# Kernel tuning notes

Hardware: AMD Instinct MI355X
Metric: run time of the kernel (lower is better)

Reference implementation:

```python
import jax, jax.numpy as jnp
import numpy as np

B, N, C = 2, 2048, 1024
H, HD = 16, 64
BASE_TEMP = 1.0


def setup_inputs() -> dict:
    key = jax.random.key(0)
    ks = jax.random.split(key, 4)
    x = jax.random.normal(ks[0], (B, N, C), dtype=jnp.float32)
    scale = jnp.asarray(HD ** (-0.5), dtype=jnp.float32)
    dynamic_temp = jnp.ones((H,), dtype=jnp.float32)
    gate_w = jax.random.normal(ks[1], (H, C), dtype=jnp.float32) * (1.0 / np.sqrt(C))
    gate_b = jnp.zeros((H,), dtype=jnp.float32)
    qkv_w = jax.random.normal(ks[2], (3 * H * HD, C), dtype=jnp.float32) * (1.0 / np.sqrt(C))
    out_w = jax.random.normal(ks[3], (C, H * HD), dtype=jnp.float32) * (1.0 / np.sqrt(H * HD))
    out_b = jnp.zeros((C,), dtype=jnp.float32)
    head_weights = jnp.ones((H,), dtype=jnp.float32) / H
    return {"x": x, "scale": scale, "dynamic_temp": dynamic_temp,
            "gate_w": gate_w, "gate_b": gate_b, "qkv_w": qkv_w,
            "out_w": out_w, "out_b": out_b, "head_weights": head_weights}


def reference(x, scale, dynamic_temp, gate_w, gate_b, qkv_w, out_w, out_b, head_weights):
    # gates: sigmoid(Linear(mean over seq)) -> [B, H]
    gates = jax.nn.sigmoid(jnp.einsum('bc,hc->bh', x.mean(axis=1), gate_w) + gate_b)
    # qkv projection (no bias): [B, N, 3*H*HD]
    qkv = jnp.einsum('bnc,oc->bno', x, qkv_w)
    q, k, v = jnp.split(qkv, 3, axis=-1)
    to_heads = lambda t: t.reshape(B, N, H, HD).transpose(0, 2, 1, 3)  # [B,H,N,HD]
    q, k, v = to_heads(q), to_heads(k), to_heads(v)
    temps = jax.nn.softplus(dynamic_temp)  # [H]
    dots = jnp.einsum('bhnd,bhmd->bhnm', q, k) * scale
    dots = dots / (temps[None, :, None, None] * BASE_TEMP)
    attn = jax.nn.softmax(dots, axis=-1)
    attn = attn * gates[:, :, None, None]  # post-softmax per-(batch,head) gate
    # dropout is identity in eval mode
    out = jnp.einsum('bhnm,bhmd->bhnd', attn, v)
    out = out.transpose(0, 2, 1, 3)  # [B,N,H,HD]
    hw = jax.nn.softmax(head_weights, axis=0)
    out = out * hw[None, None, :, None]
    out = out.reshape(B, N, H * HD)
    return jnp.einsum('bnf,cf->bnc', out, out_w) + out_b
```

## Files before the change

kernel.cpp:

```cpp
#include <hip/hip_runtime.h>

#define BB 2
#define NN 2048
#define CC 1024
#define HH 16
#define HD 64

typedef __attribute__((ext_vector_type(8))) __bf16 bf16x8;
typedef __attribute__((ext_vector_type(4))) __bf16 bf16x4;
typedef __attribute__((ext_vector_type(4))) float f32x4;

__device__ inline bf16x8 cvt8(float4 a, float4 b) {
    bf16x8 r;
    r[0] = (__bf16)a.x; r[1] = (__bf16)a.y; r[2] = (__bf16)a.z; r[3] = (__bf16)a.w;
    r[4] = (__bf16)b.x; r[5] = (__bf16)b.y; r[6] = (__bf16)b.z; r[7] = (__bf16)b.w;
    return r;
}

__device__ inline void gload16(const void* g, void* l) {
    __builtin_amdgcn_global_load_lds(
        (const __attribute__((address_space(1))) unsigned int*)g,
        (__attribute__((address_space(3))) unsigned int*)l, 16, 0, 0);
}

__global__ __launch_bounds__(256) void k_prep(const float* __restrict__ x,
        __bf16* __restrict__ xbf, float* __restrict__ partial) {
    int blk = blockIdx.x, t = threadIdx.x;
    size_t base = (size_t)blk * 16 * CC + t * 4;
    const float* xp = x + base;
    __bf16* xo = xbf + base;
    float4 s = {0.f, 0.f, 0.f, 0.f};
    #pragma unroll 4
    for (int i = 0; i < 16; ++i) {
        float4 v = *(const float4*)(xp + (size_t)i * CC);
        s.x += v.x; s.y += v.y; s.z += v.z; s.w += v.w;
        bf16x4 o;
        o[0] = (__bf16)v.x; o[1] = (__bf16)v.y; o[2] = (__bf16)v.z; o[3] = (__bf16)v.w;
        *(bf16x4*)(xo + (size_t)i * CC) = o;
    }
    *(float4*)(partial + (size_t)blk * CC + t * 4) = s;
}

__global__ __launch_bounds__(256) void k_cvt(const float* __restrict__ src,
        __bf16* __restrict__ dst, int n8) {
    int i = blockIdx.x * 256 + threadIdx.x;
    if (i >= n8) return;
    const float4* sp = (const float4*)(src + (size_t)i * 8);
    *(bf16x8*)(dst + (size_t)i * 8) = cvt8(sp[0], sp[1]);
}

__global__ __launch_bounds__(256) void k_coef(const float* __restrict__ partial,
        const float* __restrict__ gate_w, const float* __restrict__ gate_b,
        const float* __restrict__ dtemp, const float* __restrict__ hwts,
        const float* __restrict__ scale_p,
        float* __restrict__ coef, float* __restrict__ invt) {
    __shared__ float red[4];
    int p = blockIdx.x;
    int b = p >> 4, h = p & 15;
    int t = threadIdx.x;
    float acc = 0.f;
    #pragma unroll
    for (int cc = 0; cc < 4; ++cc) {
        int c = cc * 256 + t;
        float mv = 0.f;
        for (int ch = 0; ch < 128; ++ch)
            mv += partial[(size_t)(b * 128 + ch) * CC + c];
        acc += (mv * (1.f / (float)NN)) * gate_w[h * CC + c];
    }
    #pragma unroll
    for (int m = 32; m; m >>= 1) acc += __shfl_xor(acc, m);
    if ((t & 63) == 0) red[t >> 6] = acc;
    __syncthreads();
    if (t == 0) {
        float tot = red[0] + red[1] + red[2] + red[3];
        float g = 1.f / (1.f + __expf(-(tot + gate_b[h])));
        float mx = -1e30f;
        for (int i = 0; i < HH; ++i) mx = fmaxf(mx, hwts[i]);
        float s = 0.f;
        for (int i = 0; i < HH; ++i) s += __expf(hwts[i] - mx);
        float hw = __expf(hwts[h] - mx) / s;
        coef[p] = g * hw;
        if (b == 0) {
            float d = dtemp[h];
            float sp = (d > 20.f) ? d : log1pf(__expf(d));
            invt[h] = scale_p[0] / (sp * 1.0f );
        }
    }
}

template <int BM, int BN, int EPI>
__global__ __launch_bounds__(256) void k_gemm2(const __bf16* __restrict__ A,
        const __bf16* __restrict__ Bw, int K,
        __bf16* __restrict__ qo, __bf16* __restrict__ ko, __bf16* __restrict__ vto,
        const float* __restrict__ invt,
        float* __restrict__ outp, const float* __restrict__ bias) {
    constexpr int WM = BM / 2, WN = BN / 2, FM = WM / 16, FN = WN / 16;
    __shared__ __bf16 As[BM * 32];
    __shared__ __bf16 Bs[BN * 32];
    int t = threadIdx.x, lane = t & 63, w = t >> 6;
    int wr = w >> 1, wc = w & 1;
    int fr = lane & 15, kg = lane >> 4;
    int lr = lane >> 2, lc = lane & 3;
    int m0 = blockIdx.x * BM, o0 = blockIdx.y * BN;
    f32x4 acc[FM][FN] = {};
    for (int k0 = 0; k0 < K; k0 += 32) {
        __syncthreads();
        #pragma unroll
        for (int s = 0; s < BM / 64; ++s) {
            int r0 = w * (BM / 4) + s * 16;
            gload16(A + (size_t)(m0 + r0 + lr) * K + k0 + lc * 8, &As[r0 * 32]);
        }
        #pragma unroll
        for (int s = 0; s < BN / 64; ++s) {
            int r0 = w * (BN / 4) + s * 16;
            gload16(Bw + (size_t)(o0 + r0 + lr) * K + k0 + lc * 8, &Bs[r0 * 32]);
        }
        __syncthreads();
        bf16x8 av[FM], bv[FN];
        #pragma unroll
        for (int mi = 0; mi < FM; ++mi)
            av[mi] = *(const bf16x8*)&As[(wr * WM + mi * 16 + fr) * 32 + kg * 8];
        #pragma unroll
        for (int ni = 0; ni < FN; ++ni)
            bv[ni] = *(const bf16x8*)&Bs[(wc * WN + ni * 16 + fr) * 32 + kg * 8];
        #pragma unroll
        for (int mi = 0; mi < FM; ++mi)
            #pragma unroll
            for (int ni = 0; ni < FN; ++ni)
                acc[mi][ni] = __builtin_amdgcn_mfma_f32_16x16x32_bf16(av[mi], bv[ni],
                                                                      acc[mi][ni], 0, 0, 0);
    }
    #pragma unroll
    for (int mi = 0; mi < FM; ++mi)
        #pragma unroll
        for (int ni = 0; ni < FN; ++ni)
            #pragma unroll
            for (int reg = 0; reg < 4; ++reg) {
                int m = m0 + wr * WM + mi * 16 + kg * 4 + reg;
                int o = o0 + wc * WN + ni * 16 + fr;
                float val = acc[mi][ni][reg];
                if constexpr (EPI == 0) {
                    int part = o >> 10, f = o & 1023;
                    int h = f >> 6, d = f & 63;
                    int b = m >> 11, n = m & 2047;
                    if (part == 0)
                        qo[(((size_t)b * HH + h) * NN + n) * HD + d] = (__bf16)(val * invt[h]);
                    else if (part == 1)
                        ko[(((size_t)b * HH + h) * NN + n) * HD + d] = (__bf16)val;
                    else
                        vto[(((size_t)b * HH + h) * HD + d) * NN + n] = (__bf16)val;
                } else {
                    outp[(size_t)m * CC + o] = val + bias[o];
                }
            }
}

__global__ __launch_bounds__(512, 4) void k_attn(const __bf16* __restrict__ qb,
        const __bf16* __restrict__ kb, const __bf16* __restrict__ vtb,
        __bf16* __restrict__ attno, const float* __restrict__ coef,
        const float* __restrict__ invt) {
    __shared__ __bf16 Ks[2][64][64];
    __shared__ __bf16 Vs[2][64][64];
    __shared__ __bf16 Ps[8][16][72];
    int t = threadIdx.x, w = t >> 6, lane = t & 63;
    int fr = lane & 15, kg = lane >> 4;
    int qt = blockIdx.x, h = blockIdx.y, b = blockIdx.z;
    int bh = b * HH + h;
    const __bf16* kbase = kb + (size_t)bh * NN * HD;
    const __bf16* vbase = vtb + (size_t)bh * HD * NN;
    float cf = coef[bh];

    int qrow = qt * 128 + w * 16 + fr;
    const __bf16* qp = qb + (size_t)bh * NN * HD + (size_t)qrow * HD;
    bf16x8 qf0 = *(const bf16x8*)(qp + kg * 8);
    bf16x8 qf1 = *(const bf16x8*)(qp + 32 + kg * 8);

    int srow = lane >> 3;
    int ssl  = (lane & 7) ^ srow;
    int r0 = w * 8;
    int sl0 = (kg ^ (fr & 7)) * 8;
    int sl1 = ((4 | kg) ^ (fr & 7)) * 8;

    f32x4 o_acc[4] = {};
    float m_r = -INFINITY, l_r = 0.f;

    gload16(kbase + (size_t)(r0 + srow) * HD + ssl * 8, &Ks[0][r0][0]);
    gload16(vbase + (size_t)(r0 + srow) * NN + ssl * 8, &Vs[0][r0][0]);
    int cur = 0;
    for (int kt = 0; kt < NN / 64; ++kt) {
        __syncthreads();
        if (kt + 1 < NN / 64) {
            gload16(kbase + ((size_t)(kt + 1) * 64 + r0 + srow) * HD + ssl * 8,
                    &Ks[cur ^ 1][r0][0]);
            gload16(vbase + (size_t)(r0 + srow) * NN + (kt + 1) * 64 + ssl * 8,
                    &Vs[cur ^ 1][r0][0]);
        }
        f32x4 sT[4] = {};
        #pragma unroll
        for (int kk = 0; kk < 2; ++kk) {
            bf16x8 qf = kk ? qf1 : qf0;
            int sl = kk ? sl1 : sl0;
            #pragma unroll
            for (int j = 0; j < 4; ++j) {
                bf16x8 kf = *(const bf16x8*)&Ks[cur][j * 16 + fr][sl];
                sT[j] = __builtin_amdgcn_mfma_f32_16x16x32_bf16(kf, qf, sT[j], 0, 0, 0);
            }
        }
        float rm = fmaxf(fmaxf(fmaxf(sT[0][0], sT[0][1]), fmaxf(sT[0][2], sT[0][3])),
                         fmaxf(fmaxf(sT[1][0], sT[1][1]), fmaxf(sT[1][2], sT[1][3])));
        rm = fmaxf(rm, fmaxf(fmaxf(fmaxf(sT[2][0], sT[2][1]), fmaxf(sT[2][2], sT[2][3])),
                             fmaxf(fmaxf(sT[3][0], sT[3][1]), fmaxf(sT[3][2], sT[3][3]))));
        rm = fmaxf(rm, __shfl_xor(rm, 16));
        rm = fmaxf(rm, __shfl_xor(rm, 32));

        float p[4][4];
        float ts = 0.f;
        if (__any(rm > m_r + 8.f)) {
            float mn = fmaxf(m_r, rm);
            float a = __expf(m_r - mn);
            m_r = mn;
            #pragma unroll
            for (int j = 0; j < 4; ++j)
                #pragma unroll
                for (int reg = 0; reg < 4; ++reg) {
                    p[j][reg] = __expf(sT[j][reg] - mn);
                    ts += p[j][reg];
                }
            ts += __shfl_xor(ts, 16);
            ts += __shfl_xor(ts, 32);
            l_r = l_r * a + ts;
            #pragma unroll
            for (int reg = 0; reg < 4; ++reg) {
                float aq = __shfl(a, kg * 4 + reg, 16);
                #pragma unroll
                for (int j2 = 0; j2 < 4; ++j2) o_acc[j2][reg] *= aq;
            }
        } else {
            #pragma unroll
            for (int j = 0; j < 4; ++j)
                #pragma unroll
                for (int reg = 0; reg < 4; ++reg) {
                    p[j][reg] = __expf(sT[j][reg] - m_r);
                    ts += p[j][reg];
                }
            ts += __shfl_xor(ts, 16);
            ts += __shfl_xor(ts, 32);
            l_r += ts;
        }
        #pragma unroll
        for (int j = 0; j < 4; ++j) {
            bf16x4 pk;
            pk[0] = (__bf16)p[j][0]; pk[1] = (__bf16)p[j][1];
            pk[2] = (__bf16)p[j][2]; pk[3] = (__bf16)p[j][3];
            *(bf16x4*)&Ps[w][fr][j * 16 + kg * 4] = pk;
        }
        #pragma unroll
        for (int kk = 0; kk < 2; ++kk) {
            bf16x8 pf = *(const bf16x8*)&Ps[w][fr][kk * 32 + kg * 8];
            int sl = kk ? sl1 : sl0;
            #pragma unroll
            for (int j2 = 0; j2 < 4; ++j2) {
                bf16x8 vf = *(const bf16x8*)&Vs[cur][j2 * 16 + fr][sl];
                o_acc[j2] = __builtin_amdgcn_mfma_f32_16x16x32_bf16(pf, vf, o_acc[j2], 0, 0, 0);
            }
        }
        cur ^= 1;
    }
    #pragma unroll
    for (int reg = 0; reg < 4; ++reg) {
        float lq = __shfl(l_r, kg * 4 + reg, 16);
        float sc = cf / lq;
        int r = qt * 128 + w * 16 + kg * 4 + reg;
        __bf16* op = attno + ((size_t)b * NN + r) * (HH * HD) + h * HD;
        #pragma unroll
        for (int j2 = 0; j2 < 4; ++j2)
            op[j2 * 16 + fr] = (__bf16)(o_acc[j2][reg] * sc);
    }
}

extern "C" void kernel_launch(void* const* d_in, const int* in_sizes, int n_in,
                              void* d_out, int out_size, void* d_ws, size_t ws_size,
                              hipStream_t stream) {
    const float* x      = (const float*)d_in[0];
    const float* scale  = (const float*)d_in[1];
    const float* dtemp  = (const float*)d_in[2];
    const float* gate_w = (const float*)d_in[3];
    const float* gate_b = (const float*)d_in[4];
    const float* qkv_w  = (const float*)d_in[5];
    const float* out_w  = (const float*)d_in[6];
    const float* out_b  = (const float*)d_in[7];
    const float* hwts   = (const float*)d_in[8];

    char* wsb = (char*)d_ws;
    float*  partial = (float*)wsb;
    float*  coefp   = (float*)(wsb + (1u << 20));
    float*  invtp   = (float*)(wsb + (1u << 20) + 128);
    char*   regA    = wsb + (1u << 20) + 512;
    char*   regB    = regA + (8u << 20);
    const size_t HSZ = (size_t)BB * HH * NN * HD;
    __bf16* qbuf  = (__bf16*)(regB + (8u << 20));
    __bf16* kbuf  = qbuf + HSZ;
    __bf16* vtbuf = kbuf + HSZ;
    __bf16* xbf     = (__bf16*)regA;
    __bf16* outw_bf = (__bf16*)regA;
    __bf16* qkvw_bf = (__bf16*)regB;
    __bf16* attno   = (__bf16*)regB;

    k_prep<<<256, 256, 0, stream>>>(x, xbf, partial);
    k_coef<<<32, 256, 0, stream>>>(partial, gate_w, gate_b, dtemp, hwts, scale, coefp, invtp);
    k_cvt<<<1536, 256, 0, stream>>>(qkv_w, qkvw_bf, 3 * HH * HD * CC / 8);
    k_gemm2<128, 128, 0><<<dim3(32, 24), 256, 0, stream>>>(xbf, qkvw_bf, CC,
            qbuf, kbuf, vtbuf, invtp, nullptr, nullptr);
    k_cvt<<<512, 256, 0, stream>>>(out_w, outw_bf, CC * HH * HD / 8);
    k_attn<<<dim3(NN / 128, HH, BB), 512, 0, stream>>>(qbuf, kbuf, vtbuf, attno, coefp, invtp);
    k_gemm2<64, 128, 1><<<dim3(64, 8), 256, 0, stream>>>(attno, outw_bf, HH * HD,
            nullptr, nullptr, nullptr, nullptr, (float*)d_out, out_b);
}
```

Baseline: 249.1 us.

## Fuse weight conversions, double-buffer GEMM, XCD-aware block mapping, swizzle attention P

Folds both weight fp32->bf16 conversions into the prep kernel, dropping two launches. Moves the out_w bf16 copy to its own buffer so the conversion no longer has to wait for the QKV GEMM to finish with regA. Double-buffers the GEMM's LDS tiles and remaps GEMM and attention blocks so neighbouring tiles land on the same XCD for L2 reuse. It also swaps MFMA operands for V blocks so the transposed V stores coalesce along n, XOR-swizzles the P scratch instead of padding it, and defers the row-sum shuffles to the end of attention. These target launch overhead, memory stalls, L2 locality and LDS bank conflicts, at the cost of more LDS per GEMM block and more complex indexing.

```diff
diff --git a/kernel.cpp b/kernel.cpp
--- a/kernel.cpp
+++ b/kernel.cpp
@@ -24,29 +24,33 @@
 }
 
 __global__ __launch_bounds__(256) void k_prep(const float* __restrict__ x,
-        __bf16* __restrict__ xbf, float* __restrict__ partial) {
+        __bf16* __restrict__ xbf, float* __restrict__ partial,
+        const float* __restrict__ qkv_w, __bf16* __restrict__ qkvw_bf,
+        const float* __restrict__ out_w, __bf16* __restrict__ outw_bf) {
     int blk = blockIdx.x, t = threadIdx.x;
-    size_t base = (size_t)blk * 16 * CC + t * 4;
-    const float* xp = x + base;
-    __bf16* xo = xbf + base;
-    float4 s = {0.f, 0.f, 0.f, 0.f};
-    #pragma unroll 4
-    for (int i = 0; i < 16; ++i) {
-        float4 v = *(const float4*)(xp + (size_t)i * CC);
-        s.x += v.x; s.y += v.y; s.z += v.z; s.w += v.w;
-        bf16x4 o;
-        o[0] = (__bf16)v.x; o[1] = (__bf16)v.y; o[2] = (__bf16)v.z; o[3] = (__bf16)v.w;
-        *(bf16x4*)(xo + (size_t)i * CC) = o;
-    }
-    *(float4*)(partial + (size_t)blk * CC + t * 4) = s;
-}
-
-__global__ __launch_bounds__(256) void k_cvt(const float* __restrict__ src,
-        __bf16* __restrict__ dst, int n8) {
-    int i = blockIdx.x * 256 + threadIdx.x;
-    if (i >= n8) return;
-    const float4* sp = (const float4*)(src + (size_t)i * 8);
-    *(bf16x8*)(dst + (size_t)i * 8) = cvt8(sp[0], sp[1]);
+    if (blk < 256) {
+        size_t base = (size_t)blk * 16 * CC + t * 4;
+        const float* xp = x + base;
+        __bf16* xo = xbf + base;
+        float4 s = {0.f, 0.f, 0.f, 0.f};
+        #pragma unroll 4
+        for (int i = 0; i < 16; ++i) {
+            float4 v = *(const float4*)(xp + (size_t)i * CC);
+            s.x += v.x; s.y += v.y; s.z += v.z; s.w += v.w;
+            bf16x4 o;
+            o[0] = (__bf16)v.x; o[1] = (__bf16)v.y; o[2] = (__bf16)v.z; o[3] = (__bf16)v.w;
+            *(bf16x4*)(xo + (size_t)i * CC) = o;
+        }
+        *(float4*)(partial + (size_t)blk * CC + t * 4) = s;
+    } else if (blk < 1792) {
+        size_t i = (size_t)(blk - 256) * 256 + t;
+        const float4* sp = (const float4*)(qkv_w + i * 8);
+        *(bf16x8*)(qkvw_bf + i * 8) = cvt8(sp[0], sp[1]);
+    } else {
+        size_t i = (size_t)(blk - 1792) * 256 + t;
+        const float4* sp = (const float4*)(out_w + i * 8);
+        *(bf16x8*)(outw_bf + i * 8) = cvt8(sp[0], sp[1]);
+    }
 }
 
 __global__ __launch_bounds__(256) void k_coef(const float* __restrict__ partial,
@@ -88,71 +92,112 @@
     }
 }
 
-template <int BM, int BN, int EPI>
-__global__ __launch_bounds__(256) void k_gemm2(const __bf16* __restrict__ A,
+template <int BM, int BN, int GX, int GY, int SX, int SY, int EPI>
+__global__ __launch_bounds__(256, 3) void k_gemm2(const __bf16* __restrict__ A,
         const __bf16* __restrict__ Bw, int K,
         __bf16* __restrict__ qo, __bf16* __restrict__ ko, __bf16* __restrict__ vto,
         const float* __restrict__ invt,
         float* __restrict__ outp, const float* __restrict__ bias) {
     constexpr int WM = BM / 2, WN = BN / 2, FM = WM / 16, FN = WN / 16;
-    __shared__ __bf16 As[BM * 32];
-    __shared__ __bf16 Bs[BN * 32];
+    constexpr int PER = SX * SY, NSTX = GX / SX;
+    __shared__ __bf16 As[2][BM * 32];
+    __shared__ __bf16 Bs[2][BN * 32];
     int t = threadIdx.x, lane = t & 63, w = t >> 6;
     int wr = w >> 1, wc = w & 1;
     int fr = lane & 15, kg = lane >> 4;
     int lr = lane >> 2, lc = lane & 3;
-    int m0 = blockIdx.x * BM, o0 = blockIdx.y * BN;
+    int bid = blockIdx.x;
+    int xcd = bid & 7, jj = bid >> 3;
+    int st = xcd + 8 * (jj / PER);
+    int inner = jj % PER;
+    int m0 = ((st % NSTX) * SX + (inner % SX)) * BM;
+    int o0 = ((st / NSTX) * SY + (inner / SX)) * BN;
+    bool vblk = (EPI == 0) && (o0 >= 2 * HH * HD);
+
     f32x4 acc[FM][FN] = {};
-    for (int k0 = 0; k0 < K; k0 += 32) {
-        __syncthreads();
+
+    auto stage = [&](int k0, int buf) {
         #pragma unroll
         for (int s = 0; s < BM / 64; ++s) {
             int r0 = w * (BM / 4) + s * 16;
-            gload16(A + (size_t)(m0 + r0 + lr) * K + k0 + lc * 8, &As[r0 * 32]);
+            gload16(A + (size_t)(m0 + r0 + lr) * K + k0 + lc * 8, &As[buf][r0 * 32]);
         }
         #pragma unroll
         for (int s = 0; s < BN / 64; ++s) {
             int r0 = w * (BN / 4) + s * 16;
-            gload16(Bw + (size_t)(o0 + r0 + lr) * K + k0 + lc * 8, &Bs[r0 * 32]);
+            gload16(Bw + (size_t)(o0 + r0 + lr) * K + k0 + lc * 8, &Bs[buf][r0 * 32]);
+        }
+    };
+
+    stage(0, 0);
+    __syncthreads();
+    int cur = 0;
+    const int NK = K / 32;
+    for (int ks = 0; ks < NK; ++ks) {
+        if (ks + 1 < NK) stage((ks + 1) * 32, cur ^ 1);
+        bf16x8 av[FM], bv[FN];
+        #pragma unroll
+        for (int mi = 0; mi < FM; ++mi)
+            av[mi] = *(const bf16x8*)&As[cur][(wr * WM + mi * 16 + fr) * 32 + kg * 8];
+        #pragma unroll
+        for (int ni = 0; ni < FN; ++ni)
+            bv[ni] = *(const bf16x8*)&Bs[cur][(wc * WN + ni * 16 + fr) * 32 + kg * 8];
+        if (vblk) {
+            #pragma unroll
+            for (int mi = 0; mi < FM; ++mi)
+                #pragma unroll
+                for (int ni = 0; ni < FN; ++ni)
+                    acc[mi][ni] = __builtin_amdgcn_mfma_f32_16x16x32_bf16(bv[ni], av[mi],
+                                                                          acc[mi][ni], 0, 0, 0);
+        } else {
+            #pragma unroll
+            for (int mi = 0; mi < FM; ++mi)
+                #pragma unroll
+                for (int ni = 0; ni < FN; ++ni)
+                    acc[mi][ni] = __builtin_amdgcn_mfma_f32_16x16x32_bf16(av[mi], bv[ni],
+                                                                          acc[mi][ni], 0, 0, 0);
         }
         __syncthreads();
-        bf16x8 av[FM], bv[FN];
+        cur ^= 1;
+    }
+
+    if (vblk) {
         #pragma unroll
         for (int mi = 0; mi < FM; ++mi)
-            av[mi] = *(const bf16x8*)&As[(wr * WM + mi * 16 + fr) * 32 + kg * 8];
-        #pragma unroll
-        for (int ni = 0; ni < FN; ++ni)
-            bv[ni] = *(const bf16x8*)&Bs[(wc * WN + ni * 16 + fr) * 32 + kg * 8];
-        #pragma unroll
-        for (int mi = 0; mi < FM; ++mi)
             #pragma unroll
             for (int ni = 0; ni < FN; ++ni)
-                acc[mi][ni] = __builtin_amdgcn_mfma_f32_16x16x32_bf16(av[mi], bv[ni],
-                                                                      acc[mi][ni], 0, 0, 0);
-    }
-    #pragma unroll
-    for (int mi = 0; mi < FM; ++mi)
-        #pragma unroll
-        for (int ni = 0; ni < FN; ++ni)
-            #pragma unroll
-            for (int reg = 0; reg < 4; ++reg) {
-                int m = m0 + wr * WM + mi * 16 + kg * 4 + reg;
-                int o = o0 + wc * WN + ni * 16 + fr;
-                float val = acc[mi][ni][reg];
-                if constexpr (EPI == 0) {
-                    int part = o >> 10, f = o & 1023;
+                #pragma unroll
+                for (int reg = 0; reg < 4; ++reg) {
+                    int o = o0 + wc * WN + ni * 16 + kg * 4 + reg;
+                    int m = m0 + wr * WM + mi * 16 + fr;
+                    int f = o - 2 * HH * HD;
                     int h = f >> 6, d = f & 63;
                     int b = m >> 11, n = m & 2047;
-                    if (part == 0)
-                        qo[(((size_t)b * HH + h) * NN + n) * HD + d] = (__bf16)(val * invt[h]);
-                    else if (part == 1)
-                        ko[(((size_t)b * HH + h) * NN + n) * HD + d] = (__bf16)val;
-                    else
-                        vto[(((size_t)b * HH + h) * HD + d) * NN + n] = (__bf16)val;
-                } else {
-                    outp[(size_t)m * CC + o] = val + bias[o];
+                    vto[(((size_t)b * HH + h) * HD + d) * NN + n] = (__bf16)acc[mi][ni][reg];
                 }
-            }
+    } else {
+        #pragma unroll
+        for (int mi = 0; mi < FM; ++mi)
+            #pragma unroll
+            for (int ni = 0; ni < FN; ++ni)
+                #pragma unroll
+                for (int reg = 0; reg < 4; ++reg) {
+                    int m = m0 + wr * WM + mi * 16 + kg * 4 + reg;
+                    int o = o0 + wc * WN + ni * 16 + fr;
+                    float val = acc[mi][ni][reg];
+                    if constexpr (EPI == 0) {
+                        int part = o >> 10, f = o & 1023;
+                        int h = f >> 6, d = f & 63;
+                        int b = m >> 11, n = m & 2047;
+                        if (part == 0)
+                            qo[(((size_t)b * HH + h) * NN + n) * HD + d] = (__bf16)(val * invt[h]);
+                        else
+                            ko[(((size_t)b * HH + h) * NN + n) * HD + d] = (__bf16)val;
+                    } else {
+                        outp[(size_t)m * CC + o] = val + bias[o];
+                    }
+                }
+    }
 }
 
 __global__ __launch_bounds__(512, 4) void k_attn(const __bf16* __restrict__ qb,
@@ -161,11 +206,14 @@
         const float* __restrict__ invt) {
     __shared__ __bf16 Ks[2][64][64];
     __shared__ __bf16 Vs[2][64][64];
-    __shared__ __bf16 Ps[8][16][72];
+    __shared__ __bf16 Ps[8][16][64];
     int t = threadIdx.x, w = t >> 6, lane = t & 63;
     int fr = lane & 15, kg = lane >> 4;
-    int qt = blockIdx.x, h = blockIdx.y, b = blockIdx.z;
-    int bh = b * HH + h;
+    int bid = blockIdx.x;
+    int xcd = bid & 7, j0 = bid >> 3;
+    int qt = j0 & 15;
+    int bh = xcd * 4 + (j0 >> 4);
+    int h = bh & 15, b = bh >> 4;
     const __bf16* kbase = kb + (size_t)bh * NN * HD;
     const __bf16* vbase = vtb + (size_t)bh * HD * NN;
     float cf = coef[bh];
@@ -180,6 +228,7 @@
     int r0 = w * 8;
     int sl0 = (kg ^ (fr & 7)) * 8;
     int sl1 = ((4 | kg) ^ (fr & 7)) * 8;
+    char* pr = (char*)&Ps[w][fr][0];
 
     f32x4 o_acc[4] = {};
     float m_r = -INFINITY, l_r = 0.f;
@@ -226,8 +275,6 @@
                     p[j][reg] = __expf(sT[j][reg] - mn);
                     ts += p[j][reg];
                 }
-            ts += __shfl_xor(ts, 16);
-            ts += __shfl_xor(ts, 32);
             l_r = l_r * a + ts;
             #pragma unroll
             for (int reg = 0; reg < 4; ++reg) {
@@ -243,8 +290,6 @@
                     p[j][reg] = __expf(sT[j][reg] - m_r);
                     ts += p[j][reg];
                 }
-            ts += __shfl_xor(ts, 16);
-            ts += __shfl_xor(ts, 32);
             l_r += ts;
         }
         #pragma unroll
@@ -252,11 +297,11 @@
             bf16x4 pk;
             pk[0] = (__bf16)p[j][0]; pk[1] = (__bf16)p[j][1];
             pk[2] = (__bf16)p[j][2]; pk[3] = (__bf16)p[j][3];
-            *(bf16x4*)&Ps[w][fr][j * 16 + kg * 4] = pk;
+            *(bf16x4*)(pr + ((((j << 1) | (kg >> 1)) ^ (fr & 7)) << 4) + ((kg & 1) << 3)) = pk;
         }
         #pragma unroll
         for (int kk = 0; kk < 2; ++kk) {
-            bf16x8 pf = *(const bf16x8*)&Ps[w][fr][kk * 32 + kg * 8];
+            bf16x8 pf = *(const bf16x8*)(pr + ((((kk << 2) | kg) ^ (fr & 7)) << 4));
             int sl = kk ? sl1 : sl0;
             #pragma unroll
             for (int j2 = 0; j2 < 4; ++j2) {
@@ -266,9 +311,12 @@
         }
         cur ^= 1;
     }
+    float lf = l_r;
+    lf += __shfl_xor(lf, 16);
+    lf += __shfl_xor(lf, 32);
     #pragma unroll
     for (int reg = 0; reg < 4; ++reg) {
-        float lq = __shfl(l_r, kg * 4 + reg, 16);
+        float lq = __shfl(lf, kg * 4 + reg, 16);
         float sc = cf / lq;
         int r = qt * 128 + w * 16 + kg * 4 + reg;
         __bf16* op = attno + ((size_t)b * NN + r) * (HH * HD) + h * HD;
@@ -302,17 +350,16 @@
     __bf16* kbuf  = qbuf + HSZ;
     __bf16* vtbuf = kbuf + HSZ;
     __bf16* xbf     = (__bf16*)regA;
-    __bf16* outw_bf = (__bf16*)regA;
+    __bf16* outw_bf = (__bf16*)(regA + (6u << 20));
+    outw_bf = (__bf16*)((char*)vtbuf + HSZ * sizeof(__bf16));
     __bf16* qkvw_bf = (__bf16*)regB;
     __bf16* attno   = (__bf16*)regB;
 
-    k_prep<<<256, 256, 0, stream>>>(x, xbf, partial);
+    k_prep<<<2304, 256, 0, stream>>>(x, xbf, partial, qkv_w, qkvw_bf, out_w, outw_bf);
     k_coef<<<32, 256, 0, stream>>>(partial, gate_w, gate_b, dtemp, hwts, scale, coefp, invtp);
-    k_cvt<<<1536, 256, 0, stream>>>(qkv_w, qkvw_bf, 3 * HH * HD * CC / 8);
-    k_gemm2<128, 128, 0><<<dim3(32, 24), 256, 0, stream>>>(xbf, qkvw_bf, CC,
+    k_gemm2<128, 128, 32, 24, 8, 3, 0><<<768, 256, 0, stream>>>(xbf, qkvw_bf, CC,
             qbuf, kbuf, vtbuf, invtp, nullptr, nullptr);
-    k_cvt<<<512, 256, 0, stream>>>(out_w, outw_bf, CC * HH * HD / 8);
-    k_attn<<<dim3(NN / 128, HH, BB), 512, 0, stream>>>(qbuf, kbuf, vtbuf, attno, coefp, invtp);
-    k_gemm2<64, 128, 1><<<dim3(64, 8), 256, 0, stream>>>(attno, outw_bf, HH * HD,
+    k_attn<<<512, 512, 0, stream>>>(qbuf, kbuf, vtbuf, attno, coefp, invtp);
+    k_gemm2<64, 128, 64, 8, 8, 2, 1><<<512, 256, 0, stream>>>(attno, outw_bf, HH * HD,
             nullptr, nullptr, nullptr, nullptr, (float*)d_out, out_b);
 }
```

New measurement: 247.2 us. About the same (-0.8%).
